# Kernel optimization log

Measured on AMD Instinct MI355X. Metric: run time of the kernel, lower is better.

## Reference

```python
import jax, jax.numpy as jnp
import numpy as np

B, SQ, SC, DIM, H = 2, 2048, 2048, 1024, 16
HD = DIM // H  # 64
NEG = -10000.0


def setup_inputs() -> dict:
    key = jax.random.key(0)
    ks = jax.random.split(key, 12)
    x = jax.random.normal(ks[0], (B, SQ, DIM), dtype=jnp.float32)
    k_cache = jax.random.normal(ks[1], (B, SC, DIM), dtype=jnp.float32)
    v_cache = jax.random.normal(ks[2], (B, SC, DIM), dtype=jnp.float32)
    # binary additive-style mask (1 = masked), as multiplied by -10000 in forward
    mask = (jax.random.uniform(ks[3], (B, SQ, SQ + SC)) > 0.9).astype(jnp.float32)
    s = 1.0 / np.sqrt(DIM)
    Wq = jax.random.normal(ks[4], (DIM, DIM), dtype=jnp.float32) * s
    Wk = jax.random.normal(ks[5], (DIM, DIM), dtype=jnp.float32) * s
    Wv = jax.random.normal(ks[6], (DIM, DIM), dtype=jnp.float32) * s
    Wo = jax.random.normal(ks[7], (DIM, DIM), dtype=jnp.float32) * s
    bq = jnp.zeros((DIM,), jnp.float32)
    bk = jnp.zeros((DIM,), jnp.float32)
    bv = jnp.zeros((DIM,), jnp.float32)
    bo = jnp.zeros((DIM,), jnp.float32)
    return {"x": x, "k_cache": k_cache, "v_cache": v_cache, "mask": mask,
            "Wq": Wq, "bq": bq, "Wk": Wk, "bk": bk, "Wv": Wv, "bv": bv,
            "Wo": Wo, "bo": bo}


def reference(x, k_cache, v_cache, mask, Wq, bq, Wk, bk, Wv, bv, Wo, bo):
    # QKV projections (dropout is inference no-op)
    q = x @ Wq + bq                      # [B, SQ, DIM]
    k = jnp.concatenate([k_cache, x @ Wk + bk], axis=-2)  # [B, SKV, DIM]
    v = jnp.concatenate([v_cache, x @ Wv + bv], axis=-2)  # [B, SKV, DIM]
    skv = k.shape[-2]
    # split heads
    qh = q.reshape(B, SQ, H, HD).transpose(0, 2, 1, 3)    # [B, H, SQ, HD]
    kh = k.reshape(B, skv, H, HD).transpose(0, 2, 1, 3)   # [B, H, SKV, HD]
    vh = v.reshape(B, skv, H, HD).transpose(0, 2, 1, 3)   # [B, H, SKV, HD]
    scores = jnp.einsum('bhqd,bhkd->bhqk', qh, kh) / np.sqrt(HD)
    scores = scores + mask[:, None, :, :] * NEG           # additive mask
    attn = jax.nn.softmax(scores, axis=-1)
    ctx = jnp.einsum('bhqk,bhkd->bhqd', attn, vh)         # [B, H, SQ, HD]
    ctx = ctx.transpose(0, 2, 1, 3).reshape(B, SQ, DIM)
    out = ctx @ Wo + bo
    return (out, k, v)
```

## Files before the change

### kernel.cpp

```cpp
#include <hip/hip_runtime.h>
#include <hip/hip_bf16.h>

#define SQL  2048
#define SKVL 4096
#define DIML 1024

typedef __attribute__((ext_vector_type(8))) short short8;
typedef __attribute__((ext_vector_type(4))) float f32x4;

#define LOG2E 1.4426950408889634f

#define GLL16(gptr, lptr)                                        \
  __builtin_amdgcn_global_load_lds(                              \
      (const __attribute__((address_space(1))) int*)(gptr),      \
      (__attribute__((address_space(3))) int*)(lptr), 16, 0, 0)

__device__ __forceinline__ short f2s(float f) {
  return __builtin_bit_cast(short, __float2bfloat16(f));
}
__device__ __forceinline__ float s2f(short s) {
  return __bfloat162float(__builtin_bit_cast(__hip_bfloat16, s));
}

__global__ __launch_bounds__(256) void prep_kernel(
    const float* __restrict__ x, short* __restrict__ xbf,
    const float* __restrict__ W0, const float* __restrict__ W1,
    const float* __restrict__ W2, const float* __restrict__ W3,
    short* __restrict__ WT,
    const float* __restrict__ kc, const float* __restrict__ vc,
    float* __restrict__ out, short* __restrict__ Kbf,
    const float* __restrict__ mask, unsigned long long* __restrict__ maskQ)
{
  __shared__ float T[64][65];
  const int bid = blockIdx.x;
  const int t = threadIdx.x;

  if (bid < 2048) {
    const size_t i = ((size_t)bid * 256 + t) * 8;
    float4 a = *(const float4*)&x[i];
    float4 b = *(const float4*)&x[i + 4];
    short8 o;
    o[0] = f2s(a.x); o[1] = f2s(a.y); o[2] = f2s(a.z); o[3] = f2s(a.w);
    o[4] = f2s(b.x); o[5] = f2s(b.y); o[6] = f2s(b.z); o[7] = f2s(b.w);
    *(short8*)&xbf[i] = o;
  } else if (bid < 3072) {
    const int lb = bid - 2048;
    const int w = lb >> 8;
    const float* W = (w == 0) ? W0 : (w == 1) ? W1 : (w == 2) ? W2 : W3;
    short* D = WT + (size_t)w * 1048576;
    const int tile = lb & 255;
    const int r0 = (tile >> 4) * 64;
    const int c0 = (tile & 15) * 64;
    const int row = t >> 2;
    const int q = t & 3;
#pragma unroll
    for (int i = 0; i < 4; i++)
      *(float4*)&T[row][q * 16 + i * 4] =
          *(const float4*)&W[(size_t)(r0 + row) * 1024 + c0 + q * 16 + i * 4];
    __syncthreads();
    short8 o0, o1;
#pragma unroll
    for (int j = 0; j < 8; j++) {
      o0[j] = f2s(T[q * 16 + j][row]);
      o1[j] = f2s(T[q * 16 + 8 + j][row]);
    }
    *(short8*)&D[(size_t)(c0 + row) * 1024 + r0 + q * 16] = o0;
    *(short8*)&D[(size_t)(c0 + row) * 1024 + r0 + q * 16 + 8] = o1;
  } else if (bid < 7168) {
    const int idx = (bid - 3072) * 256 + t;
    const int tensor = idx >> 19;
    const int cc = idx & 524287;
    const size_t e = (size_t)cc * 8;
    const int b = (int)(e >> 21);
    const size_t rem = e & 2097151;
    const float* src = tensor ? vc : kc;
    float* dst = out + (tensor ? 12582912u : 4194304u) + (size_t)b * 4194304u + rem;
    float4 a = *(const float4*)&src[e];
    float4 bb = *(const float4*)&src[e + 4];
    *(float4*)dst = a;
    *(float4*)(dst + 4) = bb;
    if (tensor == 0) {
      short8 o;
      o[0] = f2s(a.x); o[1] = f2s(a.y); o[2] = f2s(a.z); o[3] = f2s(a.w);
      o[4] = f2s(bb.x); o[5] = f2s(bb.y); o[6] = f2s(bb.z); o[7] = f2s(bb.w);
      *(short8*)&Kbf[(size_t)b * 4194304u + rem] = o;
    }
  } else {
    const int lb = bid - 7168;
    const int ktile = lb & 63;
    const int qtile = (lb >> 6) & 31;
    const int b = lb >> 11;
    const int q0 = qtile * 64, k0 = ktile * 64;
    const int row = t >> 2;
    const int q4 = t & 3;
    const float* src = mask + (size_t)(b * SQL + q0 + row) * SKVL + k0 + q4 * 16;
#pragma unroll
    for (int i = 0; i < 4; i++)
      *(float4*)&T[row][q4 * 16 + i * 4] = *(const float4*)&src[i * 4];
    __syncthreads();
    const int wv = t >> 6, ln = t & 63;
#pragma unroll
    for (int j = 0; j < 16; j++) {
      const int qrow = wv * 16 + j;
      unsigned long long w = __ballot(T[qrow][ln] > 0.5f);
      if (ln == 0)
        maskQ[(size_t)(b * SQL + q0 + qrow) * 64 + ktile] = w;
    }
  }
}

__global__ __launch_bounds__(256) void gemm_qkv(
    const short* __restrict__ A,
    const short* __restrict__ WT,
    const float* __restrict__ bq, const float* __restrict__ bk, const float* __restrict__ bv,
    short* __restrict__ qbf,
    float* __restrict__ kout, short* __restrict__ Kbf,
    float* __restrict__ vout, float qscale)
{
  constexpr int K = 1024;
  __shared__ __align__(16) short As[128 * 32];
  __shared__ __align__(16) short Bs[128 * 32];
  const int w = blockIdx.x >> 8;
  const int bid = blockIdx.x & 255;
  const int tid = threadIdx.x;
  const int lane = tid & 63;
  const int wave = tid >> 6;
  const int nb = bid & 7;
  const int mb = bid >> 3;
  const int wm = wave >> 1;
  const int wn = wave & 1;
  const int g = lane >> 4;
  const int fr = lane & 15;

  const short* BT = WT + (size_t)w * 1048576;
  const float* bias = (w == 0) ? bq : (w == 1) ? bk : bv;

  f32x4 acc[4][4] = {};

  const int c0 = tid, c1 = tid + 256;
  const short* Ab0 = A + (size_t)(mb * 128 + (c0 >> 2)) * K + (c0 & 3) * 8;
  const short* Ab1 = A + (size_t)(mb * 128 + (c1 >> 2)) * K + (c1 & 3) * 8;
  const short* Bb0 = BT + (size_t)(nb * 128 + (c0 >> 2)) * K + (c0 & 3) * 8;
  const short* Bb1 = BT + (size_t)(nb * 128 + (c1 >> 2)) * K + (c1 & 3) * 8;

  for (int k0 = 0; k0 < K; k0 += 32) {
    __syncthreads();
    GLL16(Ab0 + k0, &As[wave * 512]);
    GLL16(Ab1 + k0, &As[2048 + wave * 512]);
    GLL16(Bb0 + k0, &Bs[wave * 512]);
    GLL16(Bb1 + k0, &Bs[2048 + wave * 512]);
    __syncthreads();
    short8 af[4], bfv[4];
#pragma unroll
    for (int m = 0; m < 4; m++)
      af[m] = *(const short8*)&As[(wm * 64 + m * 16 + fr) * 32 + g * 8];
#pragma unroll
    for (int n = 0; n < 4; n++)
      bfv[n] = *(const short8*)&Bs[(wn * 64 + n * 16 + fr) * 32 + g * 8];
#pragma unroll
    for (int m = 0; m < 4; m++)
#pragma unroll
      for (int n = 0; n < 4; n++)
        acc[m][n] = __builtin_amdgcn_mfma_f32_16x16x32_bf16(af[m], bfv[n], acc[m][n], 0, 0, 0);
  }

  const int gm = mb * 128 + wm * 64;
  const int gn = nb * 128 + wn * 64;
  float bvv[4];
#pragma unroll
  for (int n = 0; n < 4; n++) bvv[n] = bias[gn + n * 16 + fr];
#pragma unroll
  for (int m = 0; m < 4; m++) {
#pragma unroll
    for (int r = 0; r < 4; r++) {
      const int row = gm + m * 16 + g * 4 + r;
      float vals[4];
      if (w == 0) {
#pragma unroll
        for (int n = 0; n < 4; n++) vals[n] = (acc[m][n][r] + bvv[n]) * qscale;
        const int drow = (row >> 11) * 2048 + (row & 2047);
#pragma unroll
        for (int n = 0; n < 4; n++)
          qbf[(size_t)drow * 1024 + gn + n * 16 + fr] = f2s(vals[n]);
      } else {
#pragma unroll
        for (int n = 0; n < 4; n++) vals[n] = acc[m][n][r] + bvv[n];
        const int drow = (row >> 11) * 4096 + 2048 + (row & 2047);
        if (w == 1) {
#pragma unroll
          for (int n = 0; n < 4; n++) {
            kout[(size_t)drow * 1024 + gn + n * 16 + fr] = vals[n];
            Kbf[(size_t)drow * 1024 + gn + n * 16 + fr] = f2s(vals[n]);
          }
        } else {
#pragma unroll
          for (int n = 0; n < 4; n++)
            vout[(size_t)drow * 1024 + gn + n * 16 + fr] = vals[n];
        }
      }
    }
  }
}

__global__ __launch_bounds__(256) void gemm_wo(
    const short* __restrict__ A,
    const short* __restrict__ BT,
    const float* __restrict__ bias,
    float* __restrict__ Cf)
{
  constexpr int K = 1024;
  __shared__ __align__(16) short As[128 * 32];
  __shared__ __align__(16) short Bs[64 * 32];
  const int tid = threadIdx.x;
  const int lane = tid & 63;
  const int wave = tid >> 6;
  const int bid = blockIdx.x;
  const int nb = bid & 15;
  const int mb = bid >> 4;
  const int wm = wave >> 1;
  const int wn = wave & 1;
  const int g = lane >> 4;
  const int fr = lane & 15;

  f32x4 acc[4][2] = {};

  const int c0 = tid, c1 = tid + 256;
  const short* Ab0 = A + (size_t)(mb * 128 + (c0 >> 2)) * K + (c0 & 3) * 8;
  const short* Ab1 = A + (size_t)(mb * 128 + (c1 >> 2)) * K + (c1 & 3) * 8;
  const short* Bb0 = BT + (size_t)(nb * 64 + (c0 >> 2)) * K + (c0 & 3) * 8;

  for (int k0 = 0; k0 < K; k0 += 32) {
    __syncthreads();
    GLL16(Ab0 + k0, &As[wave * 512]);
    GLL16(Ab1 + k0, &As[2048 + wave * 512]);
    GLL16(Bb0 + k0, &Bs[wave * 512]);
    __syncthreads();
    short8 af[4], bfv[2];
#pragma unroll
    for (int m = 0; m < 4; m++)
      af[m] = *(const short8*)&As[(wm * 64 + m * 16 + fr) * 32 + g * 8];
#pragma unroll
    for (int n = 0; n < 2; n++)
      bfv[n] = *(const short8*)&Bs[(wn * 32 + n * 16 + fr) * 32 + g * 8];
#pragma unroll
    for (int m = 0; m < 4; m++)
#pragma unroll
      for (int n = 0; n < 2; n++)
        acc[m][n] = __builtin_amdgcn_mfma_f32_16x16x32_bf16(af[m], bfv[n], acc[m][n], 0, 0, 0);
  }

  const int gm = mb * 128 + wm * 64;
  const int gn = nb * 64 + wn * 32;
  float bv[2];
#pragma unroll
  for (int n = 0; n < 2; n++) bv[n] = bias[gn + n * 16 + fr];
#pragma unroll
  for (int m = 0; m < 4; m++) {
#pragma unroll
    for (int r = 0; r < 4; r++) {
      const int row = gm + m * 16 + g * 4 + r;
#pragma unroll
      for (int n = 0; n < 2; n++)
        Cf[(size_t)row * 1024 + gn + n * 16 + fr] = acc[m][n][r] + bv[n];
    }
  }
}

__global__ __launch_bounds__(256) void transpose_v_kernel(
    const float* __restrict__ Vf, short* __restrict__ VT)
{
  __shared__ float T[64][65];
  const int bid = blockIdx.x;
  const int kb = bid & 63;
  const int h = (bid >> 6) & 15;
  const int b = bid >> 10;
  const int kt = kb * 64;
  const int t = threadIdx.x;
  const int row = t >> 2;
  const int q = t & 3;
  const float* src = Vf + (size_t)(b * SKVL + kt + row) * DIML + h * 64 + q * 16;
#pragma unroll
  for (int i = 0; i < 4; i++)
    *(float4*)&T[row][q * 16 + i * 4] = *(const float4*)&src[i * 4];
  __syncthreads();
  short8 o0, o1;
#pragma unroll
  for (int j = 0; j < 8; j++) {
    o0[j] = f2s(T[q * 16 + j][row]);
    o1[j] = f2s(T[q * 16 + 8 + j][row]);
  }
  short* D = VT + (size_t)((b * 16 + h) * 64 + row) * SKVL + kt;
  *(short8*)&D[q * 16] = o0;
  *(short8*)&D[q * 16 + 8] = o1;
}

__global__ __launch_bounds__(512) void attn_kernel(
    const short* __restrict__ Q,
    const short* __restrict__ Kb_,
    const short* __restrict__ VT_,
    const unsigned long long* __restrict__ maskQ,
    short* __restrict__ pctx,
    float2* __restrict__ ml)
{
  __shared__ __align__(16) char LDSB[40960];
  const int tid = threadIdx.x;
  const int lane = tid & 63;
  const int wave = tid >> 6;
  const int gid = blockIdx.x;
  const int xcd = gid & 7;
  const int seq = gid >> 3;
  const int group = xcd * 8 + (seq >> 4);
  const int qbB = seq & 15;
  const int half = group & 1;
  const int bh = group >> 1;
  const int b = bh >> 4;
  const int h = bh & 15;
  const int g = lane >> 4;
  const int c = lane & 15;

  const int qbase = qbB * 128 + wave * 16;

  short8 qf[2];
  {
    const short* qp = Q + (size_t)(b * SQL + qbase + c) * DIML + h * 64 + g * 8;
    qf[0] = *(const short8*)qp;
    qf[1] = *(const short8*)(qp + 32);
  }

  short8 vone;
#pragma unroll
  for (int j = 0; j < 8; j++) vone[j] = (short)0x3F80;

  const float INIT_FREE   = -16.0f;
  const float INIT_MASKED = -10000.0f * LOG2E - 16.0f;

  f32x4 ctx[4] = {};
  f32x4 lacc = {};

  const unsigned X = (unsigned)((c & 7) << 4);
  unsigned kA  = (unsigned)(c * 128) + (((unsigned)(g * 16)) ^ X);
  unsigned vA  = 16384u + (unsigned)(c * 128) + (((unsigned)(g * 16)) ^ X);
  unsigned pw0 = 24576u + (unsigned)(wave * 2048 + c * 128) +
                 (((unsigned)(g * 8)) ^ (X & 0x10u)) + (X & 0x60u);
  unsigned pr0 = 24576u + (unsigned)(wave * 2048 + c * 128) +
                 (((unsigned)(g * 16)) ^ X);
  asm volatile("" : "+v"(kA), "+v"(vA), "+v"(pw0), "+v"(pr0));

  const int k_beg = half * (SKVL / 2);
  const int srow = lane >> 3;
  const int scol = ((lane & 7) ^ srow) * 8;
  const short* gk = Kb_ + (size_t)b * SKVL * DIML + h * 64 +
                    (size_t)(k_beg + wave * 8 + srow) * DIML + scol;
  const short* gv = VT_ + (size_t)(b * 16 + h) * 64 * SKVL +
                    (size_t)(wave * 8 + srow) * SKVL + k_beg + scol;
  const unsigned long long* mqp =
      maskQ + (size_t)(b * SQL + qbase + c) * 64 + half * 32;
  const unsigned wdst = (unsigned)(wave * 1024);

  GLL16(gk, &LDSB[wdst]);
  gk += 64 * DIML;
  unsigned long long mq_cur = *mqp++;
  __syncthreads();
  unsigned kcur = 0;

  for (int t = 0; t < (SKVL / 2) / 64; t++) {
    const unsigned long long mq_nxt = *mqp++;
    asm volatile("" ::: "memory");
    GLL16(gv, &LDSB[16384u + wdst]);
    gv += 64;
    GLL16(gk, &LDSB[(kcur ^ 8192u) + wdst]);
    gk += 64 * DIML;

    __builtin_amdgcn_s_setprio(1);
    f32x4 s[4];
#pragma unroll
    for (int n = 0; n < 4; n++) {
      const unsigned wn = (unsigned)(mq_cur >> (n * 16 + g * 4)) & 0xFu;
#pragma unroll
      for (int r = 0; r < 4; r++)
        s[n][r] = ((wn >> r) & 1u) ? INIT_MASKED : INIT_FREE;
      short8 kf0 = *(const short8*)&LDSB[kcur + kA + (unsigned)(n * 2048)];
      short8 kf1 = *(const short8*)&LDSB[kcur + (kA ^ 64u) + (unsigned)(n * 2048)];
      s[n] = __builtin_amdgcn_mfma_f32_16x16x32_bf16(kf0, qf[0], s[n], 0, 0, 0);
      s[n] = __builtin_amdgcn_mfma_f32_16x16x32_bf16(kf1, qf[1], s[n], 0, 0, 0);
    }
    __builtin_amdgcn_s_setprio(0);
#pragma unroll
    for (int n = 0; n < 4; n++) {
      const float p0 = exp2f(s[n][0]);
      const float p1 = exp2f(s[n][1]);
      const float p2 = exp2f(s[n][2]);
      const float p3 = exp2f(s[n][3]);
      unsigned lo, hi;
      asm("v_cvt_pk_bf16_f32 %0, %1, %2" : "=v"(lo) : "v"(p0), "v"(p1));
      asm("v_cvt_pk_bf16_f32 %0, %1, %2" : "=v"(hi) : "v"(p2), "v"(p3));
      *(uint2*)&LDSB[pw0 ^ (unsigned)(n * 32)] = make_uint2(lo, hi);
    }

    asm volatile("s_waitcnt vmcnt(1)" ::: "memory");
    __builtin_amdgcn_s_barrier();
    __builtin_amdgcn_sched_barrier(0);

    __builtin_amdgcn_s_setprio(1);
#pragma unroll
    for (int ks = 0; ks < 2; ks++) {
      short8 pa = *(const short8*)&LDSB[pr0 ^ (unsigned)(ks * 64)];
      lacc = __builtin_amdgcn_mfma_f32_16x16x32_bf16(pa, vone, lacc, 0, 0, 0);
#pragma unroll
      for (int d = 0; d < 4; d++) {
        short8 vfr = *(const short8*)&LDSB[(vA ^ (unsigned)(ks * 64)) + (unsigned)(d * 2048)];
        ctx[d] = __builtin_amdgcn_mfma_f32_16x16x32_bf16(pa, vfr, ctx[d], 0, 0, 0);
      }
    }
    __builtin_amdgcn_s_setprio(0);

    __syncthreads();
    kcur ^= 8192u;
    mq_cur = mq_nxt;
  }

#pragma unroll
  for (int r = 0; r < 4; r++) {
    const int rg = ((b * 16 + h) << 11) + qbase + g * 4 + r;
    const size_t base = ((size_t)half << 22) + (size_t)rg * 64;
#pragma unroll
    for (int d = 0; d < 4; d++)
      pctx[base + d * 16 + c] = f2s(ctx[d][r]);
    if (c == 0) ml[half * 65536 + rg] = make_float2(0.0f, lacc[r]);
  }
}

__global__ __launch_bounds__(256) void combine_kernel(
    const short* __restrict__ pctx, const float2* __restrict__ ml,
    short* __restrict__ ctxb)
{
  const int t = blockIdx.x * 256 + threadIdx.x;
  const int r = t >> 2;
  const int seg = (t & 3) * 16;
  const float2 ml0 = ml[r];
  const float2 ml1 = ml[65536 + r];
  const float m = fmaxf(ml0.x, ml1.x);
  const float w0 = exp2f(ml0.x - m);
  const float w1 = exp2f(ml1.x - m);
  const float inv = 1.0f / (ml0.y * w0 + ml1.y * w1);
  const short8 a0 = *(const short8*)&pctx[(size_t)r * 64 + seg];
  const short8 a1 = *(const short8*)&pctx[(size_t)r * 64 + seg + 8];
  const short8 b0 = *(const short8*)&pctx[(1ull << 22) + (size_t)r * 64 + seg];
  const short8 b1 = *(const short8*)&pctx[(1ull << 22) + (size_t)r * 64 + seg + 8];
  short8 o0, o1;
#pragma unroll
  for (int j = 0; j < 8; j++) {
    o0[j] = f2s((s2f(a0[j]) * w0 + s2f(b0[j]) * w1) * inv);
    o1[j] = f2s((s2f(a1[j]) * w0 + s2f(b1[j]) * w1) * inv);
  }
  const int b = r >> 15;
  const int h = (r >> 11) & 15;
  const int q = r & 2047;
  short* D = ctxb + (size_t)(b * 2048 + q) * 1024 + h * 64 + seg;
  *(short8*)&D[0] = o0;
  *(short8*)&D[8] = o1;
}

extern "C" void kernel_launch(void* const* d_in, const int* in_sizes, int n_in,
                              void* d_out, int out_size, void* d_ws, size_t ws_size,
                              hipStream_t stream)
{
  const float* x   = (const float*)d_in[0];
  const float* kc  = (const float*)d_in[1];
  const float* vc  = (const float*)d_in[2];
  const float* msk = (const float*)d_in[3];
  const float* Wq  = (const float*)d_in[4];
  const float* bq  = (const float*)d_in[5];
  const float* Wk  = (const float*)d_in[6];
  const float* bk  = (const float*)d_in[7];
  const float* Wv  = (const float*)d_in[8];
  const float* bv  = (const float*)d_in[9];
  const float* Wo  = (const float*)d_in[10];
  const float* bo  = (const float*)d_in[11];

  float* outf = (float*)d_out;
  float* kout = outf + 4194304;
  float* vout = outf + 12582912;

  short* ws_s  = (short*)d_ws;
  short* WT    = ws_s;
  short* xbf   = ws_s + (size_t)4 * 1048576;
  short* qbf   = ws_s + (size_t)8 * 1048576;
  short* Kbf   = ws_s + (size_t)12 * 1048576;
  short* VTb   = ws_s + (size_t)20 * 1048576;
  unsigned long long* maskQ = (unsigned long long*)(ws_s + (size_t)28 * 1048576);
  short* pctx  = ws_s + (size_t)44 * 1048576;
  float2* mlp  = (float2*)(ws_s + (size_t)52 * 1048576);
  short* ctxb  = xbf;

  const float qscale = 0.125f * LOG2E;

  prep_kernel<<<11264, 256, 0, stream>>>(x, xbf, Wq, Wk, Wv, Wo, WT,
                                         kc, vc, outf, Kbf, msk, maskQ);
  gemm_qkv<<<768, 256, 0, stream>>>(xbf, WT, bq, bk, bv, qbf, kout, Kbf, vout, qscale);
  transpose_v_kernel<<<2048, 256, 0, stream>>>(vout, VTb);
  attn_kernel<<<1024, 512, 0, stream>>>(qbf, Kbf, VTb, maskQ, pctx, mlp);
  combine_kernel<<<1024, 256, 0, stream>>>(pctx, mlp, ctxb);
  gemm_wo<<<512, 256, 0, stream>>>(ctxb, WT + 3 * 1048576, bo, outf);
}
```

Baseline: 231.3 us.

## Fuse V transpose into prep and QKV GEMM epilogue, drop transpose kernel

Removes the standalone V-transpose kernel. The cached half of V is now transposed to bf16 inside extra prep_kernel blocks reading v_cache directly. The new half is transposed through LDS in the V-projection GEMM epilogue. This avoids re-reading the fp32 V output and saves one launch, at the cost of extra syncs and LDS traffic in the GEMM epilogue and heavier prep blocks.

```diff
diff --git a/kernel.cpp b/kernel.cpp
--- a/kernel.cpp
+++ b/kernel.cpp
@@ -29,7 +29,8 @@
     short* __restrict__ WT,
     const float* __restrict__ kc, const float* __restrict__ vc,
     float* __restrict__ out, short* __restrict__ Kbf,
-    const float* __restrict__ mask, unsigned long long* __restrict__ maskQ)
+    const float* __restrict__ mask, unsigned long long* __restrict__ maskQ,
+    short* __restrict__ VTb)
 {
   __shared__ float T[64][65];
   const int bid = blockIdx.x;
@@ -85,7 +86,7 @@
       o[4] = f2s(bb.x); o[5] = f2s(bb.y); o[6] = f2s(bb.z); o[7] = f2s(bb.w);
       *(short8*)&Kbf[(size_t)b * 4194304u + rem] = o;
     }
-  } else {
+  } else if (bid < 11264) {
     const int lb = bid - 7168;
     const int ktile = lb & 63;
     const int qtile = (lb >> 6) & 31;
@@ -106,6 +107,28 @@
       if (ln == 0)
         maskQ[(size_t)(b * SQL + q0 + qrow) * 64 + ktile] = w;
     }
+  } else {
+    const int lb = bid - 11264;
+    const int kb = lb & 31;
+    const int h = (lb >> 5) & 15;
+    const int b = lb >> 9;
+    const int kt = kb * 64;
+    const int row = t >> 2;
+    const int q = t & 3;
+    const float* src = vc + (size_t)(b * 2048 + kt + row) * DIML + h * 64 + q * 16;
+#pragma unroll
+    for (int i = 0; i < 4; i++)
+      *(float4*)&T[row][q * 16 + i * 4] = *(const float4*)&src[i * 4];
+    __syncthreads();
+    short8 o0, o1;
+#pragma unroll
+    for (int j = 0; j < 8; j++) {
+      o0[j] = f2s(T[q * 16 + j][row]);
+      o1[j] = f2s(T[q * 16 + 8 + j][row]);
+    }
+    short* D = VTb + (size_t)((b * 16 + h) * 64 + row) * SKVL + kt;
+    *(short8*)&D[q * 16] = o0;
+    *(short8*)&D[q * 16 + 8] = o1;
   }
 }
 
@@ -115,7 +138,7 @@
     const float* __restrict__ bq, const float* __restrict__ bk, const float* __restrict__ bv,
     short* __restrict__ qbf,
     float* __restrict__ kout, short* __restrict__ Kbf,
-    float* __restrict__ vout, float qscale)
+    float* __restrict__ vout, short* __restrict__ VTb, float qscale)
 {
   constexpr int K = 1024;
   __shared__ __align__(16) short As[128 * 32];
@@ -198,6 +221,33 @@
             vout[(size_t)drow * 1024 + gn + n * 16 + fr] = vals[n];
         }
       }
+    }
+  }
+
+  if (w == 2) {
+    const int b2 = (mb * 128) >> 11;
+    const int tok0 = 2048 + ((mb * 128) & 2047);
+    short* Tb = As;
+    for (int ci = 0; ci < 8; ci++) {
+      __syncthreads();
+      if ((ci >> 2) == wn) {
+        const int n = ci & 3;
+#pragma unroll
+        for (int m = 0; m < 4; m++)
+#pragma unroll
+          for (int r = 0; r < 4; r++)
+            Tb[(wm * 64 + m * 16 + g * 4 + r) * 17 + fr] = f2s(acc[m][n][r] + bvv[n]);
+      }
+      __syncthreads();
+      const int dl = tid >> 4;
+      const int tk = (tid & 15) * 8;
+      short8 o;
+#pragma unroll
+      for (int j = 0; j < 8; j++) o[j] = Tb[(tk + j) * 17 + dl];
+      const int dcol = nb * 128 + ci * 16 + dl;
+      const int h2 = dcol >> 6, d2 = dcol & 63;
+      short* D = VTb + (size_t)((b2 * 16 + h2) * 64 + d2) * SKVL + tok0 + tk;
+      *(short8*)D = o;
     }
   }
 }
@@ -264,34 +314,6 @@
         Cf[(size_t)row * 1024 + gn + n * 16 + fr] = acc[m][n][r] + bv[n];
     }
   }
-}
-
-__global__ __launch_bounds__(256) void transpose_v_kernel(
-    const float* __restrict__ Vf, short* __restrict__ VT)
-{
-  __shared__ float T[64][65];
-  const int bid = blockIdx.x;
-  const int kb = bid & 63;
-  const int h = (bid >> 6) & 15;
-  const int b = bid >> 10;
-  const int kt = kb * 64;
-  const int t = threadIdx.x;
-  const int row = t >> 2;
-  const int q = t & 3;
-  const float* src = Vf + (size_t)(b * SKVL + kt + row) * DIML + h * 64 + q * 16;
-#pragma unroll
-  for (int i = 0; i < 4; i++)
-    *(float4*)&T[row][q * 16 + i * 4] = *(const float4*)&src[i * 4];
-  __syncthreads();
-  short8 o0, o1;
-#pragma unroll
-  for (int j = 0; j < 8; j++) {
-    o0[j] = f2s(T[q * 16 + j][row]);
-    o1[j] = f2s(T[q * 16 + 8 + j][row]);
-  }
-  short* D = VT + (size_t)((b * 16 + h) * 64 + row) * SKVL + kt;
-  *(short8*)&D[q * 16] = o0;
-  *(short8*)&D[q * 16 + 8] = o1;
 }
 
 __global__ __launch_bounds__(512) void attn_kernel(
@@ -495,10 +517,9 @@
 
   const float qscale = 0.125f * LOG2E;
 
-  prep_kernel<<<11264, 256, 0, stream>>>(x, xbf, Wq, Wk, Wv, Wo, WT,
-                                         kc, vc, outf, Kbf, msk, maskQ);
-  gemm_qkv<<<768, 256, 0, stream>>>(xbf, WT, bq, bk, bv, qbf, kout, Kbf, vout, qscale);
-  transpose_v_kernel<<<2048, 256, 0, stream>>>(vout, VTb);
+  prep_kernel<<<12288, 256, 0, stream>>>(x, xbf, Wq, Wk, Wv, Wo, WT,
+                                         kc, vc, outf, Kbf, msk, maskQ, VTb);
+  gemm_qkv<<<768, 256, 0, stream>>>(xbf, WT, bq, bk, bv, qbf, kout, Kbf, vout, VTb, qscale);
   attn_kernel<<<1024, 512, 0, stream>>>(qbf, Kbf, VTb, maskQ, pctx, mlp);
   combine_kernel<<<1024, 256, 0, stream>>>(pctx, mlp, ctxb);
   gemm_wo<<<512, 256, 0, stream>>>(ctxb, WT + 3 * 1048576, bo, outf);
```

New measurement: 228.0 us (median of 2 runs). About the same (-1.4%).
